# Performance work log

Hardware: AMD Instinct MI355X
Metric: run time of the kernel (lower is better)

Reference implementation:

```python
import jax, jax.numpy as jnp
import numpy as np

DT = 1.0  # module init dt

def setup_inputs() -> dict:
    key = jax.random.key(0)
    k1, k2 = jax.random.split(key)
    x = jax.random.normal(k1, (8, 4096, 512), dtype=jnp.float32)
    w = jax.random.normal(k2, (512,), dtype=jnp.float32)
    return {"x": x, "w": w}

def reference(x, w):
    # h_t = h_{t-1} + dt*(x_t - relu(w)*h_{t-1}) = a*h_{t-1} + dt*x_t,  a = 1 - dt*relu(w)
    a = (1.0 - DT * jax.nn.relu(w)).astype(x.dtype)  # [d]
    h0 = jnp.zeros((x.shape[0], x.shape[2]), dtype=x.dtype)  # [b, d]
    xt = jnp.swapaxes(x, 0, 1)  # [t, b, d]

    def step(h, x_t):
        h_next = a * h + DT * x_t
        return h_next, h_next

    _, hs = jax.lax.scan(step, h0, xt)  # [t, b, d]
    return jnp.swapaxes(hs, 0, 1)  # [b, t, d] (return_sequences=True)
```

## Files before the change

### kernel.cpp

```cpp
#include <hip/hip_runtime.h>


#define RB 8
#define RT 4096
#define RD 512
#define RC 64
#define RL 64
#define DG (RD / 4)

#define HB 1e15f

__device__ __forceinline__ float sclamp(float v) {
    return fminf(fmaxf(v, -HB), HB);
}

__global__ void __launch_bounds__(DG)
k_carry(const float4* __restrict__ x4, const float4* __restrict__ w4,
        float4* __restrict__ Lc) {
    const int g  = threadIdx.x;
    const int bc = blockIdx.x;
    const int b  = bc >> 6;
    const int c  = bc & (RC - 1);

    const float4 wv = w4[g];
    const float ax = 1.0f - fmaxf(wv.x, 0.0f);
    const float ay = 1.0f - fmaxf(wv.y, 0.0f);
    const float az = 1.0f - fmaxf(wv.z, 0.0f);
    const float aw = 1.0f - fmaxf(wv.w, 0.0f);

    const float4* __restrict__ xp = x4 + ((size_t)b * RT + (size_t)c * RL) * DG + g;

    float hx = 0.f, hy = 0.f, hz = 0.f, hw = 0.f;
#pragma unroll 8
    for (int i = 0; i < RL; ++i) {
        const float4 v = xp[(size_t)i * DG];
        hx = sclamp(ax * hx + v.x);
        hy = sclamp(ay * hy + v.y);
        hz = sclamp(az * hz + v.z);
        hw = sclamp(aw * hw + v.w);
    }
    Lc[(size_t)bc * DG + g] = make_float4(hx, hy, hz, hw);
}

__global__ void __launch_bounds__(DG)
k_final(const float4* __restrict__ x4, const float4* __restrict__ w4,
        const float4* __restrict__ Lc, float4* __restrict__ out4) {
    const int g  = threadIdx.x;
    const int bc = blockIdx.x;
    const int b  = bc >> 6;
    const int c  = bc & (RC - 1);

    const float4 wv = w4[g];
    const float ax = 1.0f - fmaxf(wv.x, 0.0f);
    const float ay = 1.0f - fmaxf(wv.y, 0.0f);
    const float az = 1.0f - fmaxf(wv.z, 0.0f);
    const float aw = 1.0f - fmaxf(wv.w, 0.0f);

    float Ax = ax, Ay = ay, Az = az, Aw = aw;
#pragma unroll
    for (int i = 0; i < 6; ++i) {
        Ax = sclamp(Ax * Ax); Ay = sclamp(Ay * Ay);
        Az = sclamp(Az * Az); Aw = sclamp(Aw * Aw);
    }

    const float4* __restrict__ lp = Lc + (size_t)b * RC * DG + g;
    float hx = 0.f, hy = 0.f, hz = 0.f, hw = 0.f;
    for (int j = 0; j < c; ++j) {
        const float4 L = lp[(size_t)j * DG];
        hx = sclamp(Ax * hx + L.x);
        hy = sclamp(Ay * hy + L.y);
        hz = sclamp(Az * hz + L.z);
        hw = sclamp(Aw * hw + L.w);
    }

    const float4* __restrict__ xp = x4   + ((size_t)b * RT + (size_t)c * RL) * DG + g;
    float4*       __restrict__ op = out4 + ((size_t)b * RT + (size_t)c * RL) * DG + g;
#pragma unroll 8
    for (int i = 0; i < RL; ++i) {
        const float4 v = xp[(size_t)i * DG];
        hx = sclamp(ax * hx + v.x);
        hy = sclamp(ay * hy + v.y);
        hz = sclamp(az * hz + v.z);
        hw = sclamp(aw * hw + v.w);
        op[(size_t)i * DG] = make_float4(hx, hy, hz, hw);
    }
}

__global__ void __launch_bounds__(256)
rnn_seq_sat(const float* __restrict__ x, const float* __restrict__ w,
            float* __restrict__ out) {
    const int idx = blockIdx.x * blockDim.x + threadIdx.x;
    if (idx >= RB * RD) return;
    const int b = idx >> 9;
    const int d = idx & (RD - 1);
    const float a = 1.0f - fmaxf(w[d], 0.0f);
    const float* xp = x + (size_t)b * RT * RD + d;
    float* op = out + (size_t)b * RT * RD + d;
    float h = 0.f;
#pragma unroll 4
    for (int t = 0; t < RT; ++t) {
        h = sclamp(a * h + xp[(size_t)t * RD]);
        op[(size_t)t * RD] = h;
    }
}

extern "C" void kernel_launch(void* const* d_in, const int* in_sizes, int n_in,
                              void* d_out, int out_size, void* d_ws, size_t ws_size,
                              hipStream_t stream) {
    const float* x = (const float*)d_in[0];
    const float* w = (const float*)d_in[1];
    float* out = (float*)d_out;

    const size_t need = (size_t)RB * RC * DG * sizeof(float4);
    if (ws_size >= need) {
        const float4* x4 = (const float4*)x;
        const float4* w4 = (const float4*)w;
        float4* Lc = (float4*)d_ws;
        k_carry<<<dim3(RB * RC), dim3(DG), 0, stream>>>(x4, w4, Lc);
        k_final<<<dim3(RB * RC), dim3(DG), 0, stream>>>(x4, w4, Lc, (float4*)out);
    } else {
        rnn_seq_sat<<<dim3((RB * RD) / 256), dim3(256), 0, stream>>>(x, w, out);
    }
}
```

Measured before the change: 128.5 us.

## Fuse carry and final passes into one cooperative kernel with grid sync

Merges the two-kernel chunked scan into a single cooperative kernel that computes per-chunk carries, does a grid-wide sync, then replays the chunk with the propagated prefix. It also halves the chunk length (doubling the chunk count to 1024 blocks) and uses nontemporal stores for the output. The aim is to remove one launch and raise parallelism. In exchange it pays for a grid barrier, a longer serial carry loop of up to 127 steps, and depends on all 1024 blocks being co-resident, falling back to two launches if the cooperative launch fails.

```diff
diff --git a/kernel.cpp b/kernel.cpp
--- a/kernel.cpp
+++ b/kernel.cpp
@@ -1,17 +1,83 @@
 #include <hip/hip_runtime.h>
+#include <hip/hip_cooperative_groups.h>
+
+namespace cg = cooperative_groups;
 
 
 #define RB 8
 #define RT 4096
 #define RD 512
-#define RC 64
-#define RL 64
+#define RC 128
+#define RL 32
+#define LOG2_RL 5
 #define DG (RD / 4)
 
 #define HB 1e15f
 
+typedef float f32x4 __attribute__((ext_vector_type(4)));
+
 __device__ __forceinline__ float sclamp(float v) {
     return fminf(fmaxf(v, -HB), HB);
+}
+
+__global__ void __launch_bounds__(DG)
+rnn_coop(const float4* __restrict__ x4, const float4* __restrict__ w4,
+         float4* __restrict__ Lc, float4* __restrict__ out4) {
+    const int g  = threadIdx.x;
+    const int bc = blockIdx.x;
+    const int b  = bc >> 7;
+    const int c  = bc & (RC - 1);
+
+    const float4 wv = w4[g];
+    const float ax = 1.0f - fmaxf(wv.x, 0.0f);
+    const float ay = 1.0f - fmaxf(wv.y, 0.0f);
+    const float az = 1.0f - fmaxf(wv.z, 0.0f);
+    const float aw = 1.0f - fmaxf(wv.w, 0.0f);
+
+    const float4* __restrict__ xp = x4 + ((size_t)b * RT + (size_t)c * RL) * DG + g;
+
+    float hx = 0.f, hy = 0.f, hz = 0.f, hw = 0.f;
+#pragma unroll 8
+    for (int i = 0; i < RL; ++i) {
+        const float4 v = xp[(size_t)i * DG];
+        hx = sclamp(ax * hx + v.x);
+        hy = sclamp(ay * hy + v.y);
+        hz = sclamp(az * hz + v.z);
+        hw = sclamp(aw * hw + v.w);
+    }
+    Lc[(size_t)bc * DG + g] = make_float4(hx, hy, hz, hw);
+
+    cg::this_grid().sync();
+
+    float Ax = ax, Ay = ay, Az = az, Aw = aw;
+#pragma unroll
+    for (int i = 0; i < LOG2_RL; ++i) {
+        Ax = sclamp(Ax * Ax); Ay = sclamp(Ay * Ay);
+        Az = sclamp(Az * Az); Aw = sclamp(Aw * Aw);
+    }
+
+    const float4* __restrict__ lp = Lc + (size_t)b * RC * DG + g;
+    hx = 0.f; hy = 0.f; hz = 0.f; hw = 0.f;
+#pragma unroll 4
+    for (int j = 0; j < c; ++j) {
+        const float4 L = lp[(size_t)j * DG];
+        hx = sclamp(Ax * hx + L.x);
+        hy = sclamp(Ay * hy + L.y);
+        hz = sclamp(Az * hz + L.z);
+        hw = sclamp(Aw * hw + L.w);
+    }
+
+    float4* __restrict__ op = out4 + ((size_t)b * RT + (size_t)c * RL) * DG + g;
+#pragma unroll 8
+    for (int i = 0; i < RL; ++i) {
+        const float4 v = xp[(size_t)i * DG];
+        hx = sclamp(ax * hx + v.x);
+        hy = sclamp(ay * hy + v.y);
+        hz = sclamp(az * hz + v.z);
+        hw = sclamp(aw * hw + v.w);
+        f32x4 o = {hx, hy, hz, hw};
+        __builtin_nontemporal_store(o, (f32x4*)&op[(size_t)i * DG]);
+    }
 }
 
 __global__ void __launch_bounds__(DG)
@@ -19,7 +85,7 @@
         float4* __restrict__ Lc) {
     const int g  = threadIdx.x;
     const int bc = blockIdx.x;
-    const int b  = bc >> 6;
+    const int b  = bc >> 7;
     const int c  = bc & (RC - 1);
 
     const float4 wv = w4[g];
@@ -47,7 +113,7 @@
         const float4* __restrict__ Lc, float4* __restrict__ out4) {
     const int g  = threadIdx.x;
     const int bc = blockIdx.x;
-    const int b  = bc >> 6;
+    const int b  = bc >> 7;
     const int c  = bc & (RC - 1);
 
     const float4 wv = w4[g];
@@ -58,13 +124,14 @@
 
     float Ax = ax, Ay = ay, Az = az, Aw = aw;
 #pragma unroll
-    for (int i = 0; i < 6; ++i) {
+    for (int i = 0; i < LOG2_RL; ++i) {
         Ax = sclamp(Ax * Ax); Ay = sclamp(Ay * Ay);
         Az = sclamp(Az * Az); Aw = sclamp(Aw * Aw);
     }
 
     const float4* __restrict__ lp = Lc + (size_t)b * RC * DG + g;
     float hx = 0.f, hy = 0.f, hz = 0.f, hw = 0.f;
+#pragma unroll 4
     for (int j = 0; j < c; ++j) {
         const float4 L = lp[(size_t)j * DG];
         hx = sclamp(Ax * hx + L.x);
@@ -116,8 +183,15 @@
         const float4* x4 = (const float4*)x;
         const float4* w4 = (const float4*)w;
         float4* Lc = (float4*)d_ws;
-        k_carry<<<dim3(RB * RC), dim3(DG), 0, stream>>>(x4, w4, Lc);
-        k_final<<<dim3(RB * RC), dim3(DG), 0, stream>>>(x4, w4, Lc, (float4*)out);
+        float4* o4 = (float4*)out;
+
+        void* args[] = { (void*)&x4, (void*)&w4, (void*)&Lc, (void*)&o4 };
+        hipError_t e = hipLaunchCooperativeKernel(
+            (const void*)rnn_coop, dim3(RB * RC), dim3(DG), args, 0, stream);
+        if (e != hipSuccess) {
+            k_carry<<<dim3(RB * RC), dim3(DG), 0, stream>>>(x4, w4, Lc);
+            k_final<<<dim3(RB * RC), dim3(DG), 0, stream>>>(x4, w4, Lc, o4);
+        }
     } else {
         rnn_seq_sat<<<dim3((RB * RD) / 256), dim3(256), 0, stream>>>(x, w, out);
     }
```

After: 232.7 us. +81.0%, slower.

## Halve chunk length, software-prefetch x loads, use nontemporal output stores

Applied to the files above, without the earlier changes.

Chunk count doubles to 128 and chunk length halves to 32, which doubles the number of blocks to 1024 for more parallelism, at the cost of a longer serial carry loop in k_final. Both kernels now explicitly double-buffer x loads in groups of 8 so the next loads overlap the dependent recurrence chain. Output writes use nontemporal stores to avoid polluting cache. The carry loop is also unrolled by 4.

```diff
diff --git a/kernel.cpp b/kernel.cpp
--- a/kernel.cpp
+++ b/kernel.cpp
@@ -4,14 +4,22 @@
 #define RB 8
 #define RT 4096
 #define RD 512
-#define RC 64
-#define RL 64
+#define RC 128
+#define RL 32
+#define LOG2_RL 5
 #define DG (RD / 4)
+#define PF 8
 
 #define HB 1e15f
 
+typedef float f32x4 __attribute__((ext_vector_type(4)));
+
 __device__ __forceinline__ float sclamp(float v) {
     return fminf(fmaxf(v, -HB), HB);
+}
+
+__device__ __forceinline__ f32x4 ld4(const float4* __restrict__ p) {
+    return *(const f32x4* __restrict__)p;
 }
 
 __global__ void __launch_bounds__(DG)
@@ -19,7 +27,7 @@
         float4* __restrict__ Lc) {
     const int g  = threadIdx.x;
     const int bc = blockIdx.x;
-    const int b  = bc >> 6;
+    const int b  = bc >> 7;
     const int c  = bc & (RC - 1);
 
     const float4 wv = w4[g];
@@ -30,14 +38,30 @@
 
     const float4* __restrict__ xp = x4 + ((size_t)b * RT + (size_t)c * RL) * DG + g;
 
+    f32x4 v[PF];
+#pragma unroll
+    for (int k = 0; k < PF; ++k) v[k] = ld4(xp + (size_t)k * DG);
+
     float hx = 0.f, hy = 0.f, hz = 0.f, hw = 0.f;
-#pragma unroll 8
-    for (int i = 0; i < RL; ++i) {
-        const float4 v = xp[(size_t)i * DG];
-        hx = sclamp(ax * hx + v.x);
-        hy = sclamp(ay * hy + v.y);
-        hz = sclamp(az * hz + v.z);
-        hw = sclamp(aw * hw + v.w);
+#pragma unroll
+    for (int base = 0; base < RL; base += PF) {
+        f32x4 n[PF];
+        if (base + PF < RL) {
+#pragma unroll
+            for (int k = 0; k < PF; ++k)
+                n[k] = ld4(xp + (size_t)(base + PF + k) * DG);
+        }
+#pragma unroll
+        for (int k = 0; k < PF; ++k) {
+            hx = sclamp(ax * hx + v[k].x);
+            hy = sclamp(ay * hy + v[k].y);
+            hz = sclamp(az * hz + v[k].z);
+            hw = sclamp(aw * hw + v[k].w);
+        }
+        if (base + PF < RL) {
+#pragma unroll
+            for (int k = 0; k < PF; ++k) v[k] = n[k];
+        }
     }
     Lc[(size_t)bc * DG + g] = make_float4(hx, hy, hz, hw);
 }
@@ -47,7 +71,7 @@
         const float4* __restrict__ Lc, float4* __restrict__ out4) {
     const int g  = threadIdx.x;
     const int bc = blockIdx.x;
-    const int b  = bc >> 6;
+    const int b  = bc >> 7;
     const int c  = bc & (RC - 1);
 
     const float4 wv = w4[g];
@@ -58,13 +82,14 @@
 
     float Ax = ax, Ay = ay, Az = az, Aw = aw;
 #pragma unroll
-    for (int i = 0; i < 6; ++i) {
+    for (int i = 0; i < LOG2_RL; ++i) {
         Ax = sclamp(Ax * Ax); Ay = sclamp(Ay * Ay);
         Az = sclamp(Az * Az); Aw = sclamp(Aw * Aw);
     }
 
     const float4* __restrict__ lp = Lc + (size_t)b * RC * DG + g;
     float hx = 0.f, hy = 0.f, hz = 0.f, hw = 0.f;
+#pragma unroll 4
     for (int j = 0; j < c; ++j) {
         const float4 L = lp[(size_t)j * DG];
         hx = sclamp(Ax * hx + L.x);
@@ -75,14 +100,32 @@
 
     const float4* __restrict__ xp = x4   + ((size_t)b * RT + (size_t)c * RL) * DG + g;
     float4*       __restrict__ op = out4 + ((size_t)b * RT + (size_t)c * RL) * DG + g;
-#pragma unroll 8
-    for (int i = 0; i < RL; ++i) {
-        const float4 v = xp[(size_t)i * DG];
-        hx = sclamp(ax * hx + v.x);
-        hy = sclamp(ay * hy + v.y);
-        hz = sclamp(az * hz + v.z);
-        hw = sclamp(aw * hw + v.w);
-        op[(size_t)i * DG] = make_float4(hx, hy, hz, hw);
+
+    f32x4 v[PF];
+#pragma unroll
+    for (int k = 0; k < PF; ++k) v[k] = ld4(xp + (size_t)k * DG);
+
+#pragma unroll
+    for (int base = 0; base < RL; base += PF) {
+        f32x4 n[PF];
+        if (base + PF < RL) {
+#pragma unroll
+            for (int k = 0; k < PF; ++k)
+                n[k] = ld4(xp + (size_t)(base + PF + k) * DG);
+        }
+#pragma unroll
+        for (int k = 0; k < PF; ++k) {
+            hx = sclamp(ax * hx + v[k].x);
+            hy = sclamp(ay * hy + v[k].y);
+            hz = sclamp(az * hz + v[k].z);
+            hw = sclamp(aw * hw + v[k].w);
+            f32x4 o = {hx, hy, hz, hw};
+            __builtin_nontemporal_store(o, (f32x4*)&op[(size_t)(base + k) * DG]);
+        }
+        if (base + PF < RL) {
+#pragma unroll
+            for (int k = 0; k < PF; ++k) v[k] = n[k];
+        }
     }
 }
 
```

Measured after the change: 124.2 us. 1.03x faster.

## Replace two-pass chunked scan with single-pass wave-shuffle parallel scan

Applied to the files above, without the earlier changes.

The carry and final kernels are replaced by one kernel. Each 256-thread block owns 16 feature columns of one batch row and walks time in 64-step chunks. Inside a chunk it does a Kogge-Stone scan over 16 timesteps with wave shuffles, then combines the four waves sequentially through shared memory and carries the state across chunks. Input x is read once instead of twice. Loads are prefetched DEPTH chunks ahead and stores are nontemporal. In exchange it needs a __syncthreads per chunk, and each wave touches only 64 contiguous bytes per timestep row, which could limit memory efficiency.

```diff
diff --git a/kernel.cpp b/kernel.cpp
--- a/kernel.cpp
+++ b/kernel.cpp
@@ -4,121 +4,130 @@
 #define RB 8
 #define RT 4096
 #define RD 512
-#define RC 64
-#define RL 64
 #define DG (RD / 4)
+#define TC 64
+#define NCH (RT / TC)
+#define DEPTH 8
+#define NOUT (NCH / DEPTH)
+#define HB 1e15f
 
-#define HB 1e15f
+typedef float f32x4 __attribute__((ext_vector_type(4)));
 
 __device__ __forceinline__ float sclamp(float v) {
     return fminf(fmaxf(v, -HB), HB);
 }
-
-__global__ void __launch_bounds__(DG)
-k_carry(const float4* __restrict__ x4, const float4* __restrict__ w4,
-        float4* __restrict__ Lc) {
-    const int g  = threadIdx.x;
-    const int bc = blockIdx.x;
-    const int b  = bc >> 6;
-    const int c  = bc & (RC - 1);
-
-    const float4 wv = w4[g];
-    const float ax = 1.0f - fmaxf(wv.x, 0.0f);
-    const float ay = 1.0f - fmaxf(wv.y, 0.0f);
-    const float az = 1.0f - fmaxf(wv.z, 0.0f);
-    const float aw = 1.0f - fmaxf(wv.w, 0.0f);
-
-    const float4* __restrict__ xp = x4 + ((size_t)b * RT + (size_t)c * RL) * DG + g;
-
-    float hx = 0.f, hy = 0.f, hz = 0.f, hw = 0.f;
-#pragma unroll 8
-    for (int i = 0; i < RL; ++i) {
-        const float4 v = xp[(size_t)i * DG];
-        hx = sclamp(ax * hx + v.x);
-        hy = sclamp(ay * hy + v.y);
-        hz = sclamp(az * hz + v.z);
-        hw = sclamp(aw * hw + v.w);
-    }
-    Lc[(size_t)bc * DG + g] = make_float4(hx, hy, hz, hw);
+__device__ __forceinline__ f32x4 sclamp4(f32x4 v) {
+    v.x = sclamp(v.x); v.y = sclamp(v.y);
+    v.z = sclamp(v.z); v.w = sclamp(v.w);
+    return v;
 }
-
-__global__ void __launch_bounds__(DG)
-k_final(const float4* __restrict__ x4, const float4* __restrict__ w4,
-        const float4* __restrict__ Lc, float4* __restrict__ out4) {
-    const int g  = threadIdx.x;
-    const int bc = blockIdx.x;
-    const int b  = bc >> 6;
-    const int c  = bc & (RC - 1);
-
-    const float4 wv = w4[g];
-    const float ax = 1.0f - fmaxf(wv.x, 0.0f);
-    const float ay = 1.0f - fmaxf(wv.y, 0.0f);
-    const float az = 1.0f - fmaxf(wv.z, 0.0f);
-    const float aw = 1.0f - fmaxf(wv.w, 0.0f);
-
-    float Ax = ax, Ay = ay, Az = az, Aw = aw;
-#pragma unroll
-    for (int i = 0; i < 6; ++i) {
-        Ax = sclamp(Ax * Ax); Ay = sclamp(Ay * Ay);
-        Az = sclamp(Az * Az); Aw = sclamp(Aw * Aw);
-    }
-
-    const float4* __restrict__ lp = Lc + (size_t)b * RC * DG + g;
-    float hx = 0.f, hy = 0.f, hz = 0.f, hw = 0.f;
-    for (int j = 0; j < c; ++j) {
-        const float4 L = lp[(size_t)j * DG];
-        hx = sclamp(Ax * hx + L.x);
-        hy = sclamp(Ay * hy + L.y);
-        hz = sclamp(Az * hz + L.z);
-        hw = sclamp(Aw * hw + L.w);
-    }
-
-    const float4* __restrict__ xp = x4   + ((size_t)b * RT + (size_t)c * RL) * DG + g;
-    float4*       __restrict__ op = out4 + ((size_t)b * RT + (size_t)c * RL) * DG + g;
-#pragma unroll 8
-    for (int i = 0; i < RL; ++i) {
-        const float4 v = xp[(size_t)i * DG];
-        hx = sclamp(ax * hx + v.x);
-        hy = sclamp(ay * hy + v.y);
-        hz = sclamp(az * hz + v.z);
-        hw = sclamp(aw * hw + v.w);
-        op[(size_t)i * DG] = make_float4(hx, hy, hz, hw);
-    }
+__device__ __forceinline__ f32x4 ld4(const float4* __restrict__ p) {
+    return *(const f32x4* __restrict__)p;
+}
+__device__ __forceinline__ f32x4 shfl4(f32x4 v, int src) {
+    f32x4 r;
+    r.x = __shfl(v.x, src, 64);
+    r.y = __shfl(v.y, src, 64);
+    r.z = __shfl(v.z, src, 64);
+    r.w = __shfl(v.w, src, 64);
+    return r;
 }
 
 __global__ void __launch_bounds__(256)
-rnn_seq_sat(const float* __restrict__ x, const float* __restrict__ w,
-            float* __restrict__ out) {
-    const int idx = blockIdx.x * blockDim.x + threadIdx.x;
-    if (idx >= RB * RD) return;
-    const int b = idx >> 9;
-    const int d = idx & (RD - 1);
-    const float a = 1.0f - fmaxf(w[d], 0.0f);
-    const float* xp = x + (size_t)b * RT * RD + d;
-    float* op = out + (size_t)b * RT * RD + d;
-    float h = 0.f;
-#pragma unroll 4
-    for (int t = 0; t < RT; ++t) {
-        h = sclamp(a * h + xp[(size_t)t * RD]);
-        op[(size_t)t * RD] = h;
+rnn_scan(const float4* __restrict__ x4, const float4* __restrict__ w4,
+         float4* __restrict__ out4) {
+    const int tid   = threadIdx.x;
+    const int g     = tid & 3;
+    const int wtt   = tid >> 2;
+    const int ttl   = wtt & 15;
+    const int wv    = tid >> 6;
+    const int lanei = tid & 63;
+
+    const int bid  = blockIdx.x;
+    const int u    = bid & 7;
+    const int half = (bid >> 3) & 1;
+    const int rest = bid >> 4;
+    const int pair = rest * 8 + u;
+    const int b    = pair >> 4;
+    const int tile = 2 * (pair & 15) + half;
+
+    const float4 wq = w4[tile * 4 + g];
+    f32x4 A1;
+    A1.x = 1.0f - fmaxf(wq.x, 0.0f);
+    A1.y = 1.0f - fmaxf(wq.y, 0.0f);
+    A1.z = 1.0f - fmaxf(wq.z, 0.0f);
+    A1.w = 1.0f - fmaxf(wq.w, 0.0f);
+    const f32x4 A2  = sclamp4(A1 * A1);
+    const f32x4 A4  = sclamp4(A2 * A2);
+    const f32x4 A8  = sclamp4(A4 * A4);
+    const f32x4 A16 = sclamp4(A8 * A8);
+
+    const int n = ttl + 1;
+    f32x4 P = {1.f, 1.f, 1.f, 1.f};
+    if (n & 1)  P = sclamp4(P * A1);
+    if (n & 2)  P = sclamp4(P * A2);
+    if (n & 4)  P = sclamp4(P * A4);
+    if (n & 8)  P = sclamp4(P * A8);
+    if (n & 16) P = sclamp4(P * A16);
+
+    __shared__ f32x4 Wl[2][4][4];
+
+    const size_t thoff = ((size_t)b * RT + wtt) * DG + (size_t)(tile * 4 + g);
+    const float4* __restrict__ xb = x4   + thoff;
+    float4*       __restrict__ ob = out4 + thoff;
+    const size_t CSTR = (size_t)TC * DG;
+
+    f32x4 pref[DEPTH];
+#pragma unroll
+    for (int s = 0; s < DEPTH; ++s) pref[s] = ld4(xb + (size_t)s * CSTR);
+
+    f32x4 H = {0.f, 0.f, 0.f, 0.f};
+
+    for (int o = 0; o < NOUT; ++o) {
+        f32x4 nxt[DEPTH];
+        const bool more = (o + 1 < NOUT);
+        if (more) {
+#pragma unroll
+            for (int s = 0; s < DEPTH; ++s)
+                nxt[s] = ld4(xb + (size_t)((o + 1) * DEPTH + s) * CSTR);
+        }
+#pragma unroll
+        for (int s = 0; s < DEPTH; ++s) {
+            f32x4 S = pref[s];
+            { f32x4 t = shfl4(S, ttl >= 1 ? lanei - 4  : lanei);
+              S = (ttl >= 1) ? sclamp4(A1 * t + S) : S; }
+            { f32x4 t = shfl4(S, ttl >= 2 ? lanei - 8  : lanei);
+              S = (ttl >= 2) ? sclamp4(A2 * t + S) : S; }
+            { f32x4 t = shfl4(S, ttl >= 4 ? lanei - 16 : lanei);
+              S = (ttl >= 4) ? sclamp4(A4 * t + S) : S; }
+            { f32x4 t = shfl4(S, ttl >= 8 ? lanei - 32 : lanei);
+              S = (ttl >= 8) ? sclamp4(A8 * t + S) : S; }
+            if (ttl == 15) Wl[s & 1][wv][g] = S;
+            __syncthreads();
+            f32x4 C = H;
+            f32x4 Cw = H;
+#pragma unroll
+            for (int j = 0; j < 4; ++j) {
+                if (j == wv) Cw = C;
+                C = sclamp4(A16 * C + Wl[s & 1][j][g]);
+            }
+            H = C;
+            f32x4 h = sclamp4(P * Cw + S);
+            __builtin_nontemporal_store(
+                h, (f32x4*)(ob + (size_t)(o * DEPTH + s) * CSTR));
+        }
+        if (more) {
+#pragma unroll
+            for (int s = 0; s < DEPTH; ++s) pref[s] = nxt[s];
+        }
     }
 }
 
 extern "C" void kernel_launch(void* const* d_in, const int* in_sizes, int n_in,
                               void* d_out, int out_size, void* d_ws, size_t ws_size,
                               hipStream_t stream) {
-    const float* x = (const float*)d_in[0];
-    const float* w = (const float*)d_in[1];
-    float* out = (float*)d_out;
-
-    const size_t need = (size_t)RB * RC * DG * sizeof(float4);
-    if (ws_size >= need) {
-        const float4* x4 = (const float4*)x;
-        const float4* w4 = (const float4*)w;
-        float4* Lc = (float4*)d_ws;
-        k_carry<<<dim3(RB * RC), dim3(DG), 0, stream>>>(x4, w4, Lc);
-        k_final<<<dim3(RB * RC), dim3(DG), 0, stream>>>(x4, w4, Lc, (float4*)out);
-    } else {
-        rnn_seq_sat<<<dim3((RB * RD) / 256), dim3(256), 0, stream>>>(x, w, out);
-    }
+    const float4* x4 = (const float4*)d_in[0];
+    const float4* w4 = (const float4*)d_in[1];
+    float4* o4 = (float4*)d_out;
+    rnn_scan<<<dim3(RB * (RD / 16)), dim3(256), 0, stream>>>(x4, w4, o4);
 }
```

Result: faster. 124.8 us (-2.9%).
